# Kernel optimization log

Hardware: AMD Instinct MI355X
Metric: run time of the kernel (lower is better)

The kernel has to match this reference:

```python
import jax, jax.numpy as jnp
import numpy as np

K, D, B, T = 512, 256, 32, 4096

def setup_inputs() -> dict:
    key = jax.random.key(0)
    k1, k2 = jax.random.split(key)
    z_e_x = jax.random.normal(k1, (B, D, T), dtype=jnp.float32)
    # nn.Embedding weight init uniform(-1/K, 1/K)
    emb_weight = jax.random.uniform(k2, (K, D), dtype=jnp.float32, minval=-1.0 / K, maxval=1.0 / K)
    return {"z_e_x": z_e_x, "emb_weight": emb_weight}

def reference(z_e_x, emb_weight):
    # forward(): permute [B,D,T] -> [B,T,D], nearest-codebook indices
    z = jnp.transpose(z_e_x, (0, 2, 1))  # [B, T, D]
    # squared L2 distances: ||z||^2 - 2 z.W^T + ||W||^2  -> [B, T, K]
    z_sq = jnp.sum(z * z, axis=-1, keepdims=True)           # [B, T, 1]
    w_sq = jnp.sum(emb_weight * emb_weight, axis=-1)        # [K]
    cross = jnp.einsum('btd,kd->btk', z, emb_weight)        # [B, T, K]
    dists = z_sq - 2.0 * cross + w_sq[None, None, :]
    latents = jnp.argmin(dists, axis=-1)                    # [B, T] int
    return latents
```

## Files before the change

kernel.cpp:

```cpp
#include <hip/hip_runtime.h>
#include <math.h>

#define NK 512
#define DD 256
#define NB 32
#define NT 4096

typedef __attribute__((ext_vector_type(8))) _Float16 f16x8;
typedef __attribute__((ext_vector_type(4))) float f32x4;

#define MARGIN 1.5e-4f
#define DCH 16
#define NCH 16
#define KPC 32
#define APAD 40

__device__ __forceinline__ unsigned short f16bits(float x) {
    _Float16 h = (_Float16)x;
    unsigned short s;
    __builtin_memcpy(&s, &h, 2);
    return s;
}

__global__ __launch_bounds__(512) void prep_kernel(const float* __restrict__ W,
                                                   unsigned short* __restrict__ Wpp,
                                                   float* __restrict__ wsq) {
    const int bx = blockIdx.x;
    const int k  = threadIdx.x;
    if (bx < NCH) {
        const int d0 = bx * DCH;
        float w[16];
        const float4* src4 = (const float4*)(W + (size_t)k * DD + d0);
        #pragma unroll
        for (int q = 0; q < 4; ++q) {
            float4 v = src4[q];
            w[4 * q + 0] = v.x; w[4 * q + 1] = v.y; w[4 * q + 2] = v.z; w[4 * q + 3] = v.w;
        }
        __align__(16) unsigned int dw[16];
        #pragma unroll
        for (int j = 0; j < 16; ++j) {
            unsigned short s = f16bits(w[j] * 4096.0f);
            dw[j] = (unsigned int)s | ((unsigned int)s << 16);
        }
        unsigned short* dst = Wpp + ((size_t)bx * 512 + k) * 32;
        #pragma unroll
        for (int j = 0; j < 4; ++j) ((int4*)dst)[j] = ((const int4*)dw)[j];
    } else {
        const float4* row = (const float4*)(W + (size_t)k * DD);
        double s = 0.0;
        #pragma unroll 8
        for (int i = 0; i < DD / 4; ++i) {
            float4 v = row[i];
            s += (double)v.x * v.x + (double)v.y * v.y + (double)v.z * v.z + (double)v.w * v.w;
        }
        wsq[k] = (float)s;
    }
}

__global__ __launch_bounds__(256, 2) void vq_phase1(const float* __restrict__ Z,
                                                    const unsigned short* __restrict__ Wpp,
                                                    const float* __restrict__ wsq,
                                                    float* __restrict__ gq1,
                                                    float* __restrict__ gq2,
                                                    int* __restrict__ gi1) {
    __shared__ __align__(16) short As[128 * APAD];
    __shared__ __align__(16) short Bs[256 * APAD];

    const int tid  = threadIdx.x;
    const int wave = tid >> 6;
    const int lane = tid & 63;
    const int lm   = lane & 15;
    const int lq   = lane >> 4;
    const int mw   = wave & 1;
    const int nw   = wave >> 1;

    const int bx = blockIdx.x;
    const int h  = bx & 1;
    const int tl = bx >> 1;
    const int b  = tl >> 5;
    const int t0 = (tl & 31) * 128;

    const int t_l = tid & 127;
    const int dg  = tid >> 7;

    const float* zcol = Z + (size_t)b * DD * NT + t0 + t_l;

    f32x4 acc[4][8];
    #pragma unroll
    for (int mt = 0; mt < 4; ++mt)
        #pragma unroll
        for (int nt = 0; nt < 8; ++nt)
            acc[mt][nt] = (f32x4){0.f, 0.f, 0.f, 0.f};

    double zacc = 0.0;

    for (int c = 0; c < NCH; ++c) {
        const int d0 = c * DCH;
        __syncthreads();

        {
            float zv[8];
            #pragma unroll
            for (int j = 0; j < 8; ++j)
                zv[j] = zcol[(size_t)(d0 + dg * 8 + j) * NT];
            #pragma unroll
            for (int j = 0; j < 8; ++j)
                zacc = fma((double)zv[j], (double)zv[j], zacc);

            __align__(16) unsigned int u[8];
            #pragma unroll
            for (int j = 0; j < 8; ++j) {
                _Float16 zh = (_Float16)zv[j];
                float rz = zv[j] - (float)zh;
                unsigned short hs, ls;
                __builtin_memcpy(&hs, &zh, 2);
                ls = f16bits(rz);
                u[j] = (unsigned int)hs | ((unsigned int)ls << 16);
            }
            int4* dst = (int4*)&As[t_l * APAD + dg * 16];
            dst[0] = ((const int4*)u)[0];
            dst[1] = ((const int4*)u)[1];
        }
        {
            const unsigned short* src = Wpp + ((size_t)c * 512 + h * 256 + tid) * 32;
            int4 v0 = ((const int4*)src)[0];
            int4 v1 = ((const int4*)src)[1];
            int4 v2 = ((const int4*)src)[2];
            int4 v3 = ((const int4*)src)[3];
            int4* bd = (int4*)&Bs[tid * APAD];
            bd[0] = v0; bd[1] = v1; bd[2] = v2; bd[3] = v3;
        }
        __syncthreads();

        f16x8 a[4], bb[8];
        #pragma unroll
        for (int mt = 0; mt < 4; ++mt)
            a[mt] = *(const f16x8*)&As[(mw * 64 + mt * 16 + lm) * APAD + lq * 8];
        #pragma unroll
        for (int nt = 0; nt < 8; ++nt)
            bb[nt] = *(const f16x8*)&Bs[(nw * 128 + nt * 16 + lm) * APAD + lq * 8];
        #pragma unroll
        for (int mt = 0; mt < 4; ++mt)
            #pragma unroll
            for (int nt = 0; nt < 8; ++nt)
                acc[mt][nt] = __builtin_amdgcn_mfma_f32_16x16x32_f16(
                    a[mt], bb[nt], acc[mt][nt], 0, 0, 0);
    }

    __syncthreads();
    double* zred = (double*)As;
    zred[dg * 128 + t_l] = zacc;
    __syncthreads();
    float* zf = (float*)Bs;
    if (tid < 128) zf[tid] = (float)(zred[tid] + zred[128 + tid]);
    __syncthreads();

    float wq[8];
    #pragma unroll
    for (int nt = 0; nt < 8; ++nt)
        wq[nt] = wsq[h * 256 + nw * 128 + nt * 16 + lm];
    const int kbase = h * 256 + nw * 128 + lm;

    float* cb1 = (float*)As;
    float* cb2 = cb1 + 256;
    int*   cbi = (int*)(cb2 + 256);

    #pragma unroll
    for (int mt = 0; mt < 4; ++mt) {
        #pragma unroll
        for (int r = 0; r < 4; ++r) {
            float zz = zf[mw * 64 + mt * 16 + lq * 4 + r];
            float q1 = INFINITY, q2 = INFINITY;
            int i1 = 0x7fffffff;
            #pragma unroll
            for (int nt = 0; nt < 8; ++nt) {
                float c2   = __fmul_rn(acc[mt][nt][r], 4.8828125e-4f);
                float dist = __fadd_rn(__fsub_rn(zz, c2), wq[nt]);
                int kk = kbase + nt * 16;
                if (dist < q1 || (dist == q1 && kk < i1)) { q2 = q1; q1 = dist; i1 = kk; }
                else if (dist < q2) q2 = dist;
            }
            #pragma unroll
            for (int mk = 1; mk <= 8; mk <<= 1) {
                float o1 = __shfl_xor(q1, mk);
                float o2 = __shfl_xor(q2, mk);
                int   oi = __shfl_xor(i1, mk);
                if (o1 < q1 || (o1 == q1 && oi < i1)) { q2 = fminf(q1, o2); q1 = o1; i1 = oi; }
                else { q2 = fminf(o1, q2); }
            }
            if (lm == 0) {
                int m = mw * 64 + mt * 16 + lq * 4 + r;
                cb1[m * 2 + nw] = q1;
                cb2[m * 2 + nw] = q2;
                cbi[m * 2 + nw] = i1;
            }
        }
    }
    __syncthreads();
    if (tid < 128) {
        float a1 = cb1[tid * 2],     a2 = cb2[tid * 2];     int ai = cbi[tid * 2];
        float b1 = cb1[tid * 2 + 1], b2 = cb2[tid * 2 + 1]; int bi = cbi[tid * 2 + 1];
        float q1, q2; int i1;
        if (b1 < a1 || (b1 == a1 && bi < ai)) { q1 = b1; i1 = bi; q2 = fminf(a1, b2); }
        else { q1 = a1; i1 = ai; q2 = fminf(b1, a2); }
        size_t bt = (size_t)b * NT + t0 + tid;
        gq1[bt * 2 + h] = q1;
        gq2[bt * 2 + h] = q2;
        gi1[bt * 2 + h] = i1;
    }
}

__global__ __launch_bounds__(256) void vq_fixmerge(const float* __restrict__ Z,
                                                   const float* __restrict__ W,
                                                   const float* __restrict__ wsq,
                                                   const float* __restrict__ gq1,
                                                   const float* __restrict__ gq2,
                                                   const int* __restrict__ gi1,
                                                   int* __restrict__ out) {
    __shared__ __align__(16) float Zs[8][256];
    __shared__ double pz[8][32];
    __shared__ float  zsqs[8];
    __shared__ int    bts[8];
    __shared__ float  rv[8][4];
    __shared__ int    ri[8][4];
    __shared__ int    lcnt;
    __shared__ int    llist[256];

    const int tid  = threadIdx.x;
    const int lane = tid & 63;
    const int wv   = tid >> 6;
    const int bt   = blockIdx.x * 256 + tid;

    if (tid == 0) lcnt = 0;
    __syncthreads();

    {
        float a1 = gq1[(size_t)bt * 2],     a2 = gq2[(size_t)bt * 2];     int ai = gi1[(size_t)bt * 2];
        float b1 = gq1[(size_t)bt * 2 + 1], b2 = gq2[(size_t)bt * 2 + 1]; int bi = gi1[(size_t)bt * 2 + 1];
        float q1, q2; int i1;
        if (b1 < a1 || (b1 == a1 && bi < ai)) { q1 = b1; i1 = bi; q2 = fminf(a1, b2); }
        else { q1 = a1; i1 = ai; q2 = fminf(b1, a2); }
        out[bt] = i1;
        if (q2 - q1 <= MARGIN) {
            int p = atomicAdd(&lcnt, 1);
            llist[p] = bt;
        }
    }
    __syncthreads();
    const int n = lcnt;

    for (int base = 0; base < n; base += 8) {
        const int m = (n - base < 8) ? (n - base) : 8;
        __syncthreads();
        if (tid < 8) bts[tid] = llist[base + ((tid < m) ? tid : 0)];
        __syncthreads();

        #pragma unroll
        for (int i = 0; i < 8; ++i) {
            if (i < m) {
                int tb = bts[i];
                int bb = tb >> 12, t = tb & 4095;
                Zs[i][tid] = Z[(size_t)bb * DD * NT + (size_t)tid * NT + t];
            }
        }
        __syncthreads();

        {
            int i = tid >> 5, seg = tid & 31;
            double s = 0.0;
            #pragma unroll
            for (int j = 0; j < 8; ++j) {
                double zz = (double)Zs[i][seg * 8 + j];
                s = fma(zz, zz, s);
            }
            pz[i][seg] = s;
        }
        __syncthreads();
        if (tid < 8) {
            double s = 0.0;
            #pragma unroll
            for (int j = 0; j < 32; ++j) s += pz[tid][j];
            zsqs[tid] = (float)s;
        }
        __syncthreads();

        float da[2][8];
        #pragma unroll
        for (int rr = 0; rr < 2; ++rr) {
            int k = tid + rr * 256;
            const float4* wr = (const float4*)(W + (size_t)k * DD);
            float a8[8];
            #pragma unroll
            for (int i = 0; i < 8; ++i) a8[i] = 0.f;
            for (int q = 0; q < 64; ++q) {
                float4 w4 = wr[q];
                #pragma unroll
                for (int i = 0; i < 8; ++i) {
                    float4 z4 = *(const float4*)&Zs[i][4 * q];
                    a8[i] = fmaf(z4.x, w4.x, a8[i]);
                    a8[i] = fmaf(z4.y, w4.y, a8[i]);
                    a8[i] = fmaf(z4.z, w4.z, a8[i]);
                    a8[i] = fmaf(z4.w, w4.w, a8[i]);
                }
            }
            float wqv = wsq[k];
            #pragma unroll
            for (int i = 0; i < 8; ++i)
                da[rr][i] = __fadd_rn(__fsub_rn(zsqs[i], __fmul_rn(2.0f, a8[i])), wqv);
        }

        #pragma unroll
        for (int i = 0; i < 8; ++i) {
            float v = da[0][i]; int ix = tid;
            if (da[1][i] < v) { v = da[1][i]; ix = tid + 256; }
            #pragma unroll
            for (int mk = 1; mk <= 32; mk <<= 1) {
                float ov = __shfl_xor(v, mk);
                int   oi = __shfl_xor(ix, mk);
                if (ov < v || (ov == v && oi < ix)) { v = ov; ix = oi; }
            }
            if (lane == 0) { rv[i][wv] = v; ri[i][wv] = ix; }
        }
        __syncthreads();
        if (tid < 8 && tid < m) {
            float v = INFINITY; int ix = 0x7fffffff;
            #pragma unroll
            for (int w = 0; w < 4; ++w) {
                if (rv[tid][w] < v || (rv[tid][w] == v && ri[tid][w] < ix)) {
                    v = rv[tid][w]; ix = ri[tid][w];
                }
            }
            out[bts[tid]] = ix;
        }
    }
}

#define BT 128
#define BK 128
#define DCHUNK 32
#define NKC (NK / BK)
#define NDC (DD / DCHUNK)
#define WSTR (BK + 4)

__global__ __launch_bounds__(256) void vq_fallback(const float* __restrict__ Z,
                                                   const float* __restrict__ W,
                                                   int* __restrict__ out) {
    __shared__ __align__(16) float Zs[DCHUNK * BT];
    __shared__ __align__(16) float Ws[DCHUNK * WSTR];
    __shared__ float wsqs[NK];

    const int tid = threadIdx.x;
    const int tx  = tid & 15;
    const int ty  = tid >> 4;
    const int b   = blockIdx.y;
    const int t0  = blockIdx.x * BT;

    for (int k = tid; k < NK; k += 256) {
        const float4* row = (const float4*)(W + (size_t)k * DD);
        double s = 0.0;
        for (int i = 0; i < DD / 4; ++i) {
            float4 v = row[i];
            s += (double)v.x * v.x + (double)v.y * v.y + (double)v.z * v.z + (double)v.w * v.w;
        }
        wsqs[k] = (float)s;
    }

    const float* Zb = Z + (size_t)b * DD * NT + t0;

    float best[8]; int bidx[8];
    #pragma unroll
    for (int a = 0; a < 8; ++a) { best[a] = INFINITY; bidx[a] = 0x7fffffff; }
    double zsqd[8];
    #pragma unroll
    for (int a = 0; a < 8; ++a) zsqd[a] = 0.0;
    float zsqf[8];

    for (int kc = 0; kc < NKC; ++kc) {
        float acc[8][8];
        #pragma unroll
        for (int a = 0; a < 8; ++a)
            #pragma unroll
            for (int c = 0; c < 8; ++c) acc[a][c] = 0.f;

        for (int dc = 0; dc < NDC; ++dc) {
            const int d0 = dc * DCHUNK;
            __syncthreads();
            #pragma unroll
            for (int i = 0; i < 4; ++i) {
                int f  = tid + i * 256;
                int r  = f >> 5;
                int c4 = f & 31;
                float4 v = *(const float4*)(Zb + (size_t)(d0 + r) * NT + c4 * 4);
                *(float4*)(&Zs[r * BT + c4 * 4]) = v;
            }
            #pragma unroll
            for (int i = 0; i < 4; ++i) {
                int u  = tid + i * 256;
                int k  = u >> 3;
                int rg = u & 7;
                float4 v = *(const float4*)(W + (size_t)(kc * BK + k) * DD + d0 + rg * 4);
                Ws[(rg * 4 + 0) * WSTR + k] = v.x;
                Ws[(rg * 4 + 1) * WSTR + k] = v.y;
                Ws[(rg * 4 + 2) * WSTR + k] = v.z;
                Ws[(rg * 4 + 3) * WSTR + k] = v.w;
            }
            __syncthreads();
            #pragma unroll 4
            for (int d = 0; d < DCHUNK; ++d) {
                float4 z0 = *(const float4*)(&Zs[d * BT + ty * 8]);
                float4 z1 = *(const float4*)(&Zs[d * BT + ty * 8 + 4]);
                float4 w0 = *(const float4*)(&Ws[d * WSTR + tx * 8]);
                float4 w1 = *(const float4*)(&Ws[d * WSTR + tx * 8 + 4]);
                float za[8] = {z0.x, z0.y, z0.z, z0.w, z1.x, z1.y, z1.z, z1.w};
                float wa[8] = {w0.x, w0.y, w0.z, w0.w, w1.x, w1.y, w1.z, w1.w};
                if (kc == 0) {
                    #pragma unroll
                    for (int a = 0; a < 8; ++a)
                        zsqd[a] = fma((double)za[a], (double)za[a], zsqd[a]);
                }
                #pragma unroll
                for (int a = 0; a < 8; ++a)
                    #pragma unroll
                    for (int c = 0; c < 8; ++c)
                        acc[a][c] = fmaf(za[a], wa[c], acc[a][c]);
            }
        }
        if (kc == 0) {
            #pragma unroll
            for (int a = 0; a < 8; ++a) zsqf[a] = (float)zsqd[a];
        }
        #pragma unroll
        for (int c = 0; c < 8; ++c) {
            int   kg = kc * BK + tx * 8 + c;
            float wqv = wsqs[kg];
            #pragma unroll
            for (int a = 0; a < 8; ++a) {
                float c2   = __fmul_rn(2.0f, acc[a][c]);
                float s    = __fsub_rn(zsqf[a], c2);
                float dist = __fadd_rn(s, wqv);
                if (dist < best[a] || (dist == best[a] && kg < bidx[a])) {
                    best[a] = dist; bidx[a] = kg;
                }
            }
        }
    }
    __syncthreads();
    float* redv = Zs;
    int*   redi = (int*)Ws;
    #pragma unroll
    for (int a = 0; a < 8; ++a) {
        int tl2 = ty * 8 + a;
        redv[tl2 * 16 + tx] = best[a];
        redi[tl2 * 16 + tx] = bidx[a];
    }
    __syncthreads();
    if (tid < BT) {
        float bv = INFINITY; int bi = 0x7fffffff;
        #pragma unroll
        for (int j = 0; j < 16; ++j) {
            float v = redv[tid * 16 + j];
            int   i = redi[tid * 16 + j];
            if (v < bv || (v == bv && i < bi)) { bv = v; bi = i; }
        }
        out[(size_t)b * NT + t0 + tid] = bi;
    }
}

extern "C" void kernel_launch(void* const* d_in, const int* in_sizes, int n_in,
                              void* d_out, int out_size, void* d_ws, size_t ws_size,
                              hipStream_t stream) {
    const float* Z = (const float*)d_in[0];
    const float* W = (const float*)d_in[1];
    int* out = (int*)d_out;

    const size_t OFF_WSQ = 0;
    const size_t OFF_WPP = 2048;
    const size_t OFF_GQ1 = OFF_WPP + 524288;
    const size_t OFF_GQ2 = OFF_GQ1 + 1048576;
    const size_t OFF_GI1 = OFF_GQ2 + 1048576;
    const size_t NEED    = OFF_GI1 + 1048576;

    if (ws_size >= NEED) {
        float* wsq = (float*)((char*)d_ws + OFF_WSQ);
        unsigned short* wpp = (unsigned short*)((char*)d_ws + OFF_WPP);
        float* gq1 = (float*)((char*)d_ws + OFF_GQ1);
        float* gq2 = (float*)((char*)d_ws + OFF_GQ2);
        int*   gi1 = (int*)((char*)d_ws + OFF_GI1);

        prep_kernel<<<dim3(NCH + 1), dim3(512), 0, stream>>>(W, wpp, wsq);
        vq_phase1<<<dim3(2048), dim3(256), 0, stream>>>(Z, wpp, wsq, gq1, gq2, gi1);
        vq_fixmerge<<<dim3(512), dim3(256), 0, stream>>>(Z, W, wsq, gq1, gq2, gi1, out);
    } else {
        vq_fallback<<<dim3(NT / BT, NB), dim3(256), 0, stream>>>(Z, W, out);
    }
}
```

Before: 391.4 us.

## Cover full codebook per block with double-buffered LDS and global tie list

Phase1 now runs 512-thread blocks that each cover all 512 codes, so Z is loaded and split into fp16 hi/lo once instead of twice. The chunk loop double-buffers A/B tiles in LDS, prefetching the next chunk's global loads while MFMAs run on the current one, which drops one barrier per iteration. Argmin and the top-2 margin merge move into phase1, which writes the output directly and appends near-tie rows to a compact global list via an atomic counter. The fix kernel then only grid-strides over that list, removing the gq1/gq2/gi1 round trip. The cost is higher register and LDS pressure per block and an extra atomic.

```diff
diff --git a/kernel.cpp b/kernel.cpp
--- a/kernel.cpp
+++ b/kernel.cpp
@@ -12,7 +12,6 @@
 #define MARGIN 1.5e-4f
 #define DCH 16
 #define NCH 16
-#define KPC 32
 #define APAD 40
 
 __device__ __forceinline__ unsigned short f16bits(float x) {
@@ -24,7 +23,8 @@
 
 __global__ __launch_bounds__(512) void prep_kernel(const float* __restrict__ W,
                                                    unsigned short* __restrict__ Wpp,
-                                                   float* __restrict__ wsq) {
+                                                   float* __restrict__ wsq,
+                                                   int* __restrict__ gcnt) {
     const int bx = blockIdx.x;
     const int k  = threadIdx.x;
     if (bx < NCH) {
@@ -54,17 +54,24 @@
             s += (double)v.x * v.x + (double)v.y * v.y + (double)v.z * v.z + (double)v.w * v.w;
         }
         wsq[k] = (float)s;
+        if (k == 0) *gcnt = 0;
     }
 }
 
-__global__ __launch_bounds__(256, 2) void vq_phase1(const float* __restrict__ Z,
+__global__ __launch_bounds__(512, 2) void vq_phase1(const float* __restrict__ Z,
                                                     const unsigned short* __restrict__ Wpp,
                                                     const float* __restrict__ wsq,
-                                                    float* __restrict__ gq1,
-                                                    float* __restrict__ gq2,
-                                                    int* __restrict__ gi1) {
-    __shared__ __align__(16) short As[128 * APAD];
-    __shared__ __align__(16) short Bs[256 * APAD];
+                                                    int* __restrict__ out,
+                                                    int* __restrict__ gties,
+                                                    int* __restrict__ gcnt) {
+    __shared__ __align__(16) short As[2][128 * APAD];
+    __shared__ __align__(16) short Bs[2][512 * APAD];
+    __shared__ double zred[512];
+    __shared__ float  zf[128];
+    __shared__ float  cb1[512], cb2[512];
+    __shared__ int    cbi[512];
+    __shared__ int    llist[128];
+    __shared__ int    lcnt, gbase;
 
     const int tid  = threadIdx.x;
     const int wave = tid >> 6;
@@ -75,15 +82,16 @@
     const int nw   = wave >> 1;
 
     const int bx = blockIdx.x;
-    const int h  = bx & 1;
-    const int tl = bx >> 1;
-    const int b  = tl >> 5;
-    const int t0 = (tl & 31) * 128;
+    const int b  = bx >> 5;
+    const int t0 = (bx & 31) * 128;
 
     const int t_l = tid & 127;
     const int dg  = tid >> 7;
 
     const float* zcol = Z + (size_t)b * DD * NT + t0 + t_l;
+    const unsigned short* wrow = Wpp + (size_t)tid * 32;
+
+    if (tid == 0) lcnt = 0;
 
     f32x4 acc[4][8];
     #pragma unroll
@@ -94,76 +102,93 @@
 
     double zacc = 0.0;
 
+    {
+        float zv[4];
+        #pragma unroll
+        for (int j = 0; j < 4; ++j)
+            zv[j] = zcol[(size_t)(dg * 4 + j) * NT];
+        int4 wv[4];
+        const int4* ws4 = (const int4*)wrow;
+        #pragma unroll
+        for (int q = 0; q < 4; ++q) wv[q] = ws4[q];
+
+        #pragma unroll
+        for (int j = 0; j < 4; ++j) zacc = fma((double)zv[j], (double)zv[j], zacc);
+        __align__(16) unsigned int u[4];
+        #pragma unroll
+        for (int j = 0; j < 4; ++j) {
+            _Float16 zh = (_Float16)zv[j];
+            float rz = zv[j] - (float)zh;
+            unsigned short hs, ls;
+            __builtin_memcpy(&hs, &zh, 2);
+            ls = f16bits(rz);
+            u[j] = (unsigned int)hs | ((unsigned int)ls << 16);
+        }
+        *(int4*)&As[0][t_l * APAD + dg * 8] = *(const int4*)u;
+        int4* bd = (int4*)&Bs[0][tid * APAD];
+        bd[0] = wv[0]; bd[1] = wv[1]; bd[2] = wv[2]; bd[3] = wv[3];
+    }
+    __syncthreads();
+
     for (int c = 0; c < NCH; ++c) {
-        const int d0 = c * DCH;
-        __syncthreads();
-
-        {
-            float zv[8];
-            #pragma unroll
-            for (int j = 0; j < 8; ++j)
-                zv[j] = zcol[(size_t)(d0 + dg * 8 + j) * NT];
-            #pragma unroll
-            for (int j = 0; j < 8; ++j)
-                zacc = fma((double)zv[j], (double)zv[j], zacc);
-
-            __align__(16) unsigned int u[8];
-            #pragma unroll
-            for (int j = 0; j < 8; ++j) {
-                _Float16 zh = (_Float16)zv[j];
-                float rz = zv[j] - (float)zh;
+        const int cur = c & 1;
+
+        float zv2[4]; int4 wv2[4];
+        if (c < NCH - 1) {
+            const int d0 = (c + 1) * DCH;
+            #pragma unroll
+            for (int j = 0; j < 4; ++j)
+                zv2[j] = zcol[(size_t)(d0 + dg * 4 + j) * NT];
+            const int4* ws4 = (const int4*)(wrow + (size_t)(c + 1) * NK * 32);
+            #pragma unroll
+            for (int q = 0; q < 4; ++q) wv2[q] = ws4[q];
+        }
+
+        f16x8 a[4], bb[8];
+        #pragma unroll
+        for (int mt = 0; mt < 4; ++mt)
+            a[mt] = *(const f16x8*)&As[cur][(mw * 64 + mt * 16 + lm) * APAD + lq * 8];
+        #pragma unroll
+        for (int nt = 0; nt < 8; ++nt)
+            bb[nt] = *(const f16x8*)&Bs[cur][(nw * 128 + nt * 16 + lm) * APAD + lq * 8];
+        #pragma unroll
+        for (int mt = 0; mt < 4; ++mt)
+            #pragma unroll
+            for (int nt = 0; nt < 8; ++nt)
+                acc[mt][nt] = __builtin_amdgcn_mfma_f32_16x16x32_f16(
+                    a[mt], bb[nt], acc[mt][nt], 0, 0, 0);
+
+        if (c < NCH - 1) {
+            #pragma unroll
+            for (int j = 0; j < 4; ++j) zacc = fma((double)zv2[j], (double)zv2[j], zacc);
+            __align__(16) unsigned int u[4];
+            #pragma unroll
+            for (int j = 0; j < 4; ++j) {
+                _Float16 zh = (_Float16)zv2[j];
+                float rz = zv2[j] - (float)zh;
                 unsigned short hs, ls;
                 __builtin_memcpy(&hs, &zh, 2);
                 ls = f16bits(rz);
                 u[j] = (unsigned int)hs | ((unsigned int)ls << 16);
             }
-            int4* dst = (int4*)&As[t_l * APAD + dg * 16];
-            dst[0] = ((const int4*)u)[0];
-            dst[1] = ((const int4*)u)[1];
-        }
-        {
-            const unsigned short* src = Wpp + ((size_t)c * 512 + h * 256 + tid) * 32;
-            int4 v0 = ((const int4*)src)[0];
-            int4 v1 = ((const int4*)src)[1];
-            int4 v2 = ((const int4*)src)[2];
-            int4 v3 = ((const int4*)src)[3];
-            int4* bd = (int4*)&Bs[tid * APAD];
-            bd[0] = v0; bd[1] = v1; bd[2] = v2; bd[3] = v3;
-        }
-        __syncthreads();
-
-        f16x8 a[4], bb[8];
-        #pragma unroll
-        for (int mt = 0; mt < 4; ++mt)
-            a[mt] = *(const f16x8*)&As[(mw * 64 + mt * 16 + lm) * APAD + lq * 8];
-        #pragma unroll
-        for (int nt = 0; nt < 8; ++nt)
-            bb[nt] = *(const f16x8*)&Bs[(nw * 128 + nt * 16 + lm) * APAD + lq * 8];
-        #pragma unroll
-        for (int mt = 0; mt < 4; ++mt)
-            #pragma unroll
-            for (int nt = 0; nt < 8; ++nt)
-                acc[mt][nt] = __builtin_amdgcn_mfma_f32_16x16x32_f16(
-                    a[mt], bb[nt], acc[mt][nt], 0, 0, 0);
-    }
-
-    __syncthreads();
-    double* zred = (double*)As;
+            *(int4*)&As[cur ^ 1][t_l * APAD + dg * 8] = *(const int4*)u;
+            int4* bd = (int4*)&Bs[cur ^ 1][tid * APAD];
+            bd[0] = wv2[0]; bd[1] = wv2[1]; bd[2] = wv2[2]; bd[3] = wv2[3];
+            __syncthreads();
+        }
+    }
+
     zred[dg * 128 + t_l] = zacc;
     __syncthreads();
-    float* zf = (float*)Bs;
-    if (tid < 128) zf[tid] = (float)(zred[tid] + zred[128 + tid]);
+    if (tid < 128)
+        zf[tid] = (float)(((zred[tid] + zred[128 + tid]) + zred[256 + tid]) + zred[384 + tid]);
     __syncthreads();
 
     float wq[8];
     #pragma unroll
     for (int nt = 0; nt < 8; ++nt)
-        wq[nt] = wsq[h * 256 + nw * 128 + nt * 16 + lm];
-    const int kbase = h * 256 + nw * 128 + lm;
-
-    float* cb1 = (float*)As;
-    float* cb2 = cb1 + 256;
-    int*   cbi = (int*)(cb2 + 256);
+        wq[nt] = wsq[nw * 128 + nt * 16 + lm];
+    const int kbase = nw * 128 + lm;
 
     #pragma unroll
     for (int mt = 0; mt < 4; ++mt) {
@@ -190,69 +215,57 @@
             }
             if (lm == 0) {
                 int m = mw * 64 + mt * 16 + lq * 4 + r;
-                cb1[m * 2 + nw] = q1;
-                cb2[m * 2 + nw] = q2;
-                cbi[m * 2 + nw] = i1;
+                cb1[m * 4 + nw] = q1;
+                cb2[m * 4 + nw] = q2;
+                cbi[m * 4 + nw] = i1;
             }
         }
     }
     __syncthreads();
     if (tid < 128) {
-        float a1 = cb1[tid * 2],     a2 = cb2[tid * 2];     int ai = cbi[tid * 2];
-        float b1 = cb1[tid * 2 + 1], b2 = cb2[tid * 2 + 1]; int bi = cbi[tid * 2 + 1];
-        float q1, q2; int i1;
-        if (b1 < a1 || (b1 == a1 && bi < ai)) { q1 = b1; i1 = bi; q2 = fminf(a1, b2); }
-        else { q1 = a1; i1 = ai; q2 = fminf(b1, a2); }
-        size_t bt = (size_t)b * NT + t0 + tid;
-        gq1[bt * 2 + h] = q1;
-        gq2[bt * 2 + h] = q2;
-        gi1[bt * 2 + h] = i1;
-    }
+        float q1 = cb1[tid * 4], q2 = cb2[tid * 4];
+        int   i1 = cbi[tid * 4];
+        #pragma unroll
+        for (int p = 1; p < 4; ++p) {
+            float c1 = cb1[tid * 4 + p], c2v = cb2[tid * 4 + p];
+            int   ci = cbi[tid * 4 + p];
+            if (c1 < q1 || (c1 == q1 && ci < i1)) { q2 = fminf(q1, c2v); q1 = c1; i1 = ci; }
+            else { q2 = fminf(q2, c1); }
+        }
+        out[(size_t)b * NT + t0 + tid] = i1;
+        if (q2 - q1 <= MARGIN) {
+            int p = atomicAdd(&lcnt, 1);
+            llist[p] = b * NT + t0 + tid;
+        }
+    }
+    __syncthreads();
+    if (tid == 0) gbase = (lcnt > 0) ? atomicAdd(gcnt, lcnt) : 0;
+    __syncthreads();
+    if (tid < lcnt) gties[gbase + tid] = llist[tid];
 }
 
-__global__ __launch_bounds__(256) void vq_fixmerge(const float* __restrict__ Z,
-                                                   const float* __restrict__ W,
-                                                   const float* __restrict__ wsq,
-                                                   const float* __restrict__ gq1,
-                                                   const float* __restrict__ gq2,
-                                                   const int* __restrict__ gi1,
-                                                   int* __restrict__ out) {
+__global__ __launch_bounds__(256) void vq_fix(const float* __restrict__ Z,
+                                              const float* __restrict__ W,
+                                              const float* __restrict__ wsq,
+                                              const int* __restrict__ gties,
+                                              const int* __restrict__ gcnt,
+                                              int* __restrict__ out) {
     __shared__ __align__(16) float Zs[8][256];
     __shared__ double pz[8][32];
     __shared__ float  zsqs[8];
     __shared__ int    bts[8];
     __shared__ float  rv[8][4];
     __shared__ int    ri[8][4];
-    __shared__ int    lcnt;
-    __shared__ int    llist[256];
 
     const int tid  = threadIdx.x;
     const int lane = tid & 63;
-    const int wv   = tid >> 6;
-    const int bt   = blockIdx.x * 256 + tid;
-
-    if (tid == 0) lcnt = 0;
-    __syncthreads();
-
-    {
-        float a1 = gq1[(size_t)bt * 2],     a2 = gq2[(size_t)bt * 2];     int ai = gi1[(size_t)bt * 2];
-        float b1 = gq1[(size_t)bt * 2 + 1], b2 = gq2[(size_t)bt * 2 + 1]; int bi = gi1[(size_t)bt * 2 + 1];
-        float q1, q2; int i1;
-        if (b1 < a1 || (b1 == a1 && bi < ai)) { q1 = b1; i1 = bi; q2 = fminf(a1, b2); }
-        else { q1 = a1; i1 = ai; q2 = fminf(b1, a2); }
-        out[bt] = i1;
-        if (q2 - q1 <= MARGIN) {
-            int p = atomicAdd(&lcnt, 1);
-            llist[p] = bt;
-        }
-    }
-    __syncthreads();
-    const int n = lcnt;
-
-    for (int base = 0; base < n; base += 8) {
+    const int wvx  = tid >> 6;
+    const int n    = *gcnt;
+
+    for (int base = blockIdx.x * 8; base < n; base += (int)gridDim.x * 8) {
         const int m = (n - base < 8) ? (n - base) : 8;
         __syncthreads();
-        if (tid < 8) bts[tid] = llist[base + ((tid < m) ? tid : 0)];
+        if (tid < 8) bts[tid] = gties[base + ((tid < m) ? tid : 0)];
         __syncthreads();
 
         #pragma unroll
@@ -292,6 +305,7 @@
             float a8[8];
             #pragma unroll
             for (int i = 0; i < 8; ++i) a8[i] = 0.f;
+            #pragma unroll 2
             for (int q = 0; q < 64; ++q) {
                 float4 w4 = wr[q];
                 #pragma unroll
@@ -319,7 +333,7 @@
                 int   oi = __shfl_xor(ix, mk);
                 if (ov < v || (ov == v && oi < ix)) { v = ov; ix = oi; }
             }
-            if (lane == 0) { rv[i][wv] = v; ri[i][wv] = ix; }
+            if (lane == 0) { rv[i][wvx] = v; ri[i][wvx] = ix; }
         }
         __syncthreads();
         if (tid < 8 && tid < m) {
@@ -474,22 +488,20 @@
     int* out = (int*)d_out;
 
     const size_t OFF_WSQ = 0;
-    const size_t OFF_WPP = 2048;
-    const size_t OFF_GQ1 = OFF_WPP + 524288;
-    const size_t OFF_GQ2 = OFF_GQ1 + 1048576;
-    const size_t OFF_GI1 = OFF_GQ2 + 1048576;
-    const size_t NEED    = OFF_GI1 + 1048576;
+    const size_t OFF_CNT = 2048;
+    const size_t OFF_WPP = 4096;
+    const size_t OFF_TIE = OFF_WPP + 524288;
+    const size_t NEED    = OFF_TIE + 524288;
 
     if (ws_size >= NEED) {
         float* wsq = (float*)((char*)d_ws + OFF_WSQ);
+        int*   gcnt = (int*)((char*)d_ws + OFF_CNT);
         unsigned short* wpp = (unsigned short*)((char*)d_ws + OFF_WPP);
-        float* gq1 = (float*)((char*)d_ws + OFF_GQ1);
-        float* gq2 = (float*)((char*)d_ws + OFF_GQ2);
-        int*   gi1 = (int*)((char*)d_ws + OFF_GI1);
-
-        prep_kernel<<<dim3(NCH + 1), dim3(512), 0, stream>>>(W, wpp, wsq);
-        vq_phase1<<<dim3(2048), dim3(256), 0, stream>>>(Z, wpp, wsq, gq1, gq2, gi1);
-        vq_fixmerge<<<dim3(512), dim3(256), 0, stream>>>(Z, W, wsq, gq1, gq2, gi1, out);
+        int*   gties = (int*)((char*)d_ws + OFF_TIE);
+
+        prep_kernel<<<dim3(NCH + 1), dim3(512), 0, stream>>>(W, wpp, wsq, gcnt);
+        vq_phase1<<<dim3(1024), dim3(512), 0, stream>>>(Z, wpp, wsq, out, gties, gcnt);
+        vq_fix<<<dim3(256), dim3(256), 0, stream>>>(Z, W, wsq, gties, gcnt, out);
     } else {
         vq_fallback<<<dim3(NT / BT, NB), dim3(256), 0, stream>>>(Z, W, out);
     }
```

After: 374.7 us. 1.04x faster.
